# Kernel optimization log

Hardware: AMD Instinct MI355X
Metric: run time of the kernel (lower is better)

Reference implementation:

```python
import jax, jax.numpy as jnp
import numpy as np

N, D = 1024, 256


def setup_inputs() -> dict:
    key = jax.random.key(0)
    k1, k2 = jax.random.split(key)
    mu_X = jax.random.normal(k1, (N, D), dtype=jnp.float32)
    log_sigma = jax.random.normal(k2, (N, D), dtype=jnp.float32)
    return {"mu_X": mu_X, "log_sigma": log_sigma}


def reference(mu_X, log_sigma):
    # F.normalize: x / max(||x||_2, eps), eps=1e-12
    norm = jnp.linalg.norm(mu_X, axis=-1, keepdims=True)
    mu = mu_X / jnp.maximum(norm, 1e-12)
    sigma_sq = jnp.exp(log_sigma)                       # [N, D]
    sig_sum = sigma_sq[:, None, :] + sigma_sq[None, :, :]  # [N, N, D]
    # pairwise squared diff weighted by summed variances + log-variance penalty
    diff = (mu[:, None, :] - mu[None, :, :]) ** 2 / (1e-10 + sig_sum) + jnp.log(sig_sum)
    return -diff.sum(axis=2)                            # [N, N]
```

## Files before the change

### kernel.cpp

```cpp
#include <hip/hip_runtime.h>

#define N 1024
#define D 256

#define RI 8
#define LDW 260

__global__ __launch_bounds__(256) void prep3(
    const float* __restrict__ muX, const float* __restrict__ ls,
    float2* __restrict__ msT2) {
  const int i0 = blockIdx.x * RI;
  const int t = threadIdx.x;
  __shared__ float smu[RI][LDW];
  __shared__ float ssg[RI][LDW];
  __shared__ float sred[RI][32];
  __shared__ float rden[RI];
  const float4* mu4 = (const float4*)(muX + (size_t)i0 * D);
  const float4* ls4 = (const float4*)(ls + (size_t)i0 * D);
#pragma unroll
  for (int u = 0; u < 2; ++u) {
    const int idx = u * 256 + t;
    const int row = idx >> 6, c4 = idx & 63;
    const float4 v = mu4[idx];
    *(float4*)&smu[row][c4 * 4] = v;
    const float4 e = ls4[idx];
    float4 x;
    x.x = __expf(e.x) + 5e-11f; x.y = __expf(e.y) + 5e-11f;
    x.z = __expf(e.z) + 5e-11f; x.w = __expf(e.w) + 5e-11f;
    *(float4*)&ssg[row][c4 * 4] = x;
  }
  __syncthreads();
  {
    const int r = t >> 5, q = t & 31;
    float s = 0.f;
#pragma unroll
    for (int k = 0; k < 8; ++k) {
      const float v = smu[r][q + 32 * k];
      s = fmaf(v, v, s);
    }
    sred[r][q] = s;
  }
  __syncthreads();
  if (t < RI) {
    float tot = 0.f;
    for (int u = 0; u < 32; ++u) tot += sred[t][u];
    rden[t] = 1.0f / fmaxf(sqrtf(tot), 1e-12f);
  }
  __syncthreads();
#pragma unroll
  for (int pass = 0; pass < 8; ++pass) {
    const int f = pass * 256 + t;
    const int b = f & 1, il = (f >> 1) & 7, g = f >> 4;
    const int d = 2 * g + b;
    msT2[((size_t)g * N + i0 + il) * 2 + b] =
        make_float2(smu[il][d] * rden[il], ssg[il][d]);
  }
}

__global__ __launch_bounds__(128) void pair_kernel(
    const float4* __restrict__ msT4, float* __restrict__ out) {
  int L = blockIdx.x;
  int js = 0, base = 0;
  while (L >= base + 64 * (js + 1)) { base += 64 * (js + 1); ++js; }
  const int ib = L - base;
  const int j0 = js * 128, i0 = ib * 2;
  const bool diag = (ib >= js * 64);
  const int j = j0 + threadIdx.x;

  float acc[2] = {0.f, 0.f};
  float p[2] = {1.f, 1.f};
  int ea[2] = {0, 0};

#pragma unroll 4
  for (int g = 0; g < D / 2; ++g) {
    const float4 jv = msT4[(size_t)g * N + j];
#pragma unroll
    for (int k = 0; k < 2; ++k) {
      const float4 iv = msT4[(size_t)g * N + i0 + k];
      {
        const float sv = iv.y + jv.y;
        const float t0 = iv.x - jv.x;
        acc[k] = fmaf(t0 * t0, __builtin_amdgcn_rcpf(sv), acc[k]);
        p[k] *= sv;
      }
      {
        const float sv = iv.w + jv.w;
        const float t0 = iv.z - jv.z;
        acc[k] = fmaf(t0 * t0, __builtin_amdgcn_rcpf(sv), acc[k]);
        p[k] *= sv;
      }
    }
    if (g & 1) {
#pragma unroll
      for (int k = 0; k < 2; ++k) {
        const int bb = __float_as_int(p[k]);
        ea[k] += bb >> 23;
        p[k] = __int_as_float((bb & 0x007fffff) | 0x3f800000);
      }
    }
  }

  constexpr float LN2 = 0.6931471805599453f;
  float v[2];
#pragma unroll
  for (int k = 0; k < 2; ++k) {
    const float lg2 = (float)(ea[k] - 127 * (D / 4)) + __log2f(p[k]);
    v[k] = -(acc[k] + LN2 * lg2);
  }

  if (!diag) {
    out[(size_t)i0 * N + j] = v[0];
    out[(size_t)(i0 + 1) * N + j] = v[1];
    *(float2*)(out + (size_t)j * N + i0) = make_float2(v[0], v[1]);
  } else {
#pragma unroll
    for (int k = 0; k < 2; ++k) {
      const int i = i0 + k;
      if (j >= i) out[(size_t)i * N + j] = v[k];
      if (j > i) out[(size_t)j * N + i] = v[k];
    }
  }
}

extern "C" void kernel_launch(void* const* d_in, const int* in_sizes, int n_in,
                              void* d_out, int out_size, void* d_ws, size_t ws_size,
                              hipStream_t stream) {
  const float* muX = (const float*)d_in[0];
  const float* ls  = (const float*)d_in[1];
  float* out = (float*)d_out;
  float2* msT2 = (float2*)d_ws;
  prep3<<<dim3(N / RI), dim3(256), 0, stream>>>(muX, ls, msT2);
  const int nblocks = 64 * (8 * 9 / 2);
  pair_kernel<<<dim3(nblocks), dim3(128), 0, stream>>>((const float4*)msT2,
                                                       out);
}
```

Measured before the change: 95.72 us.

## Combine four reciprocals into one via common-denominator fraction summation

```diff
diff --git a/kernel.cpp b/kernel.cpp
--- a/kernel.cpp
+++ b/kernel.cpp
@@ -51,9 +51,10 @@
   for (int pass = 0; pass < 8; ++pass) {
     const int f = pass * 256 + t;
     const int b = f & 1, il = (f >> 1) & 7, g = f >> 4;
-    const int d = 2 * g + b;
+    const float* src = b ? &ssg[il][0] : &smu[il][0];
+    const float sc = b ? 1.0f : rden[il];
     msT2[((size_t)g * N + i0 + il) * 2 + b] =
-        make_float2(smu[il][d] * rden[il], ssg[il][d]);
+        make_float2(src[2 * g] * sc, src[2 * g + 1] * sc);
   }
 }
 
@@ -72,25 +73,28 @@
   int ea[2] = {0, 0};
 
 #pragma unroll 4
-  for (int g = 0; g < D / 2; ++g) {
-    const float4 jv = msT4[(size_t)g * N + j];
+  for (int gg = 0; gg < D / 4; ++gg) {
+    const float4 jva = msT4[(size_t)(2 * gg) * N + j];
+    const float4 jvb = msT4[(size_t)(2 * gg + 1) * N + j];
 #pragma unroll
     for (int k = 0; k < 2; ++k) {
-      const float4 iv = msT4[(size_t)g * N + i0 + k];
-      {
-        const float sv = iv.y + jv.y;
-        const float t0 = iv.x - jv.x;
-        acc[k] = fmaf(t0 * t0, __builtin_amdgcn_rcpf(sv), acc[k]);
-        p[k] *= sv;
-      }
-      {
-        const float sv = iv.w + jv.w;
-        const float t0 = iv.z - jv.z;
-        acc[k] = fmaf(t0 * t0, __builtin_amdgcn_rcpf(sv), acc[k]);
-        p[k] *= sv;
-      }
+      const float4 iva = msT4[(size_t)(2 * gg) * N + i0 + k];
+      const float4 ivb = msT4[(size_t)(2 * gg + 1) * N + i0 + k];
+      const float sa0 = iva.z + jva.z, sa1 = iva.w + jva.w;
+      const float da0 = iva.x - jva.x, da1 = iva.y - jva.y;
+      const float sb0 = ivb.z + jvb.z, sb1 = ivb.w + jvb.w;
+      const float db0 = ivb.x - jvb.x, db1 = ivb.y - jvb.y;
+      const float qa0 = da0 * da0, qa1 = da1 * da1;
+      const float qb0 = db0 * db0, qb1 = db1 * db1;
+      const float s01 = sa0 * sa1, s23 = sb0 * sb1;
+      float na = qa0 * sa1; na = fmaf(qa1, sa0, na);
+      float nb = qb0 * sb1; nb = fmaf(qb1, sb0, nb);
+      float num = na * s23; num = fmaf(nb, s01, num);
+      const float den = s01 * s23;
+      acc[k] = fmaf(num, __builtin_amdgcn_rcpf(den), acc[k]);
+      p[k] *= den;
     }
-    if (g & 1) {
+    if (gg & 1) {
 #pragma unroll
       for (int k = 0; k < 2; ++k) {
         const int bb = __float_as_int(p[k]);
@@ -104,7 +108,7 @@
   float v[2];
 #pragma unroll
   for (int k = 0; k < 2; ++k) {
-    const float lg2 = (float)(ea[k] - 127 * (D / 4)) + __log2f(p[k]);
+    const float lg2 = (float)(ea[k] - 127 * (D / 8)) + __log2f(p[k]);
     v[k] = -(acc[k] + LN2 * lg2);
   }
 
```

After: 91.64 us. -4.3%, faster.
